# Optimization experiments

Measured on AMD Instinct MI355X. Metric: run time of the kernel, lower is better.

Reference implementation:

```python
import jax, jax.numpy as jnp
import numpy as np

B, N, E, H = 4, 512, 512, 8   # batch, tokens, embedding_channels (=KV_size_S), num_heads
C = 4 * E                      # KV_size_C
D = E // H                     # head dim
EPS = 1e-5                     # InstanceNorm2d default eps


def _inorm(x, axes):
    # InstanceNorm2d (affine=False): normalize over spatial axes with biased variance
    m = jnp.mean(x, axis=axes, keepdims=True)
    v = jnp.var(x, axis=axes, keepdims=True)
    return (x - m) * jax.lax.rsqrt(v + EPS)


def setup_inputs() -> dict:
    key = jax.random.key(0)
    ks = jax.random.split(key, 24)
    s = 0.02
    inp = {
        'emb1': jax.random.normal(ks[0], (B, N, E), jnp.float32),
        'emb2': jax.random.normal(ks[1], (B, N, E), jnp.float32),
        'emb3': jax.random.normal(ks[2], (B, N, E), jnp.float32),
        'emb4': jax.random.normal(ks[3], (B, N, E), jnp.float32),
        'emb_C': jax.random.normal(ks[4], (B, N, C), jnp.float32),
        'Wq1': jax.random.normal(ks[5], (E, E), jnp.float32) * s,
        'Wq2': jax.random.normal(ks[6], (E, E), jnp.float32) * s,
        'Wq3': jax.random.normal(ks[7], (E, E), jnp.float32) * s,
        'Wq4': jax.random.normal(ks[8], (E, E), jnp.float32) * s,
        'Wk': jax.random.normal(ks[9], (E, E), jnp.float32) * s,
        'Wv': jax.random.normal(ks[10], (E, E), jnp.float32) * s,
        'WqC': jax.random.normal(ks[11], (C, C), jnp.float32) * s,
        'WkC': jax.random.normal(ks[12], (C, C), jnp.float32) * s,
        'WvC': jax.random.normal(ks[13], (C, C), jnp.float32) * s,
        'Wo1': jax.random.normal(ks[14], (E, E), jnp.float32) * s,
        'Wo2': jax.random.normal(ks[15], (E, E), jnp.float32) * s,
        'Wo3': jax.random.normal(ks[16], (E, E), jnp.float32) * s,
        'Wo4': jax.random.normal(ks[17], (E, E), jnp.float32) * s,
    }
    return inp


def _heads(x):
    # [B, N, E] -> [B, H, N, D]
    b, n, _ = x.shape
    return x.reshape(b, n, H, D).transpose(0, 2, 1, 3)


def reference(emb1, emb2, emb3, emb4, emb_C,
              Wq1, Wq2, Wq3, Wq4, Wk, Wv, WqC, WkC, WvC,
              Wo1, Wo2, Wo3, Wo4):
    # ---- channel cross-attention ----
    QC = emb_C @ WqC.T            # [B, N, C]
    KC = emb_C @ WkC.T
    VC = emb_C @ WvC.T
    attn_c = jnp.einsum('bnc,bnd->bcd', QC, KC)        # [B, C, C]
    sim_c = jax.nn.softmax(_inorm(attn_c, (1, 2)), axis=-1)  # psi1 + softmax(dim=3)
    ctx_c = jnp.einsum('bcd,bnd->bcn', sim_c, VC)      # [B, C, N]
    T_hat = ctx_c.transpose(0, 2, 1)                   # [B, N, C]
    # split last dim into 4 chunks of E, concat along tokens -> [B, 4N, E]
    KV_S = jnp.concatenate(jnp.split(T_hat, 4, axis=2), axis=1)

    # ---- spatial multi-head cross-attention, shared K/V ----
    K = _heads(KV_S @ Wk.T)       # [B, H, 4N, D]
    V = _heads(KV_S @ Wv.T)

    outs = []
    for emb, Wq, Wo in ((emb1, Wq1, Wo1), (emb2, Wq2, Wo2),
                        (emb3, Wq3, Wo3), (emb4, Wq4, Wo4)):
        Q = _heads(emb @ Wq.T)                          # [B, H, N, D]
        attn = jnp.einsum('bhnd,bhmd->bhnm', Q, K)      # [B, H, N, 4N]
        sim = jax.nn.softmax(_inorm(attn, (2, 3)), axis=-1)  # psi2 + softmax
        ctx = jnp.einsum('bhnm,bhmd->bhnd', sim, V)     # [B, H, N, D]
        ctx = ctx.transpose(0, 2, 1, 3).reshape(emb.shape[0], emb.shape[1], E)
        outs.append(ctx @ Wo.T)
    return tuple(outs)
```

## Files before the change

### kernel.cpp

```cpp
#include <hip/hip_runtime.h>
#include <hip/hip_bf16.h>
#include <hip/hip_fp16.h>

typedef long long i64;
typedef unsigned int u32;
typedef __attribute__((ext_vector_type(8))) short bf16x8;
typedef __attribute__((ext_vector_type(4))) float f32x4;

#define MFMA_BF16 __builtin_amdgcn_mfma_f32_16x16x32_bf16

__device__ __forceinline__ void glds16(const void* g, void* l){
    __builtin_amdgcn_global_load_lds((const __attribute__((address_space(1))) u32*)g,
                                     (__attribute__((address_space(3))) u32*)l, 16, 0, 0);
}
__device__ __forceinline__ void split1(float x, ushort& h, ushort& l){
    unsigned b = __float_as_uint(x);
    h = (ushort)(b >> 16);
    float hf = __uint_as_float(b & 0xFFFF0000u);
    float lf = x - hf;
    l = (ushort)(__float_as_uint(lf) >> 16);
}
__device__ __forceinline__ float bfpair(ushort h, ushort l){
    return __uint_as_float((u32)h << 16) + __uint_as_float((u32)l << 16);
}
__device__ __forceinline__ void ld4h(const __half* p, float v[4]){
    const __half2* q = (const __half2*)p;
    __half2 a = q[0], b = q[1];
    v[0]=__low2float(a); v[1]=__high2float(a);
    v[2]=__low2float(b); v[3]=__high2float(b);
}
__device__ __forceinline__ bf16x8 fragS(const ushort* P, int row, int g){
    return *(const bf16x8*)&P[row*64 + (((g) ^ (row & 7)) << 3)];
}

struct P4 { const void* p[4]; };
struct I4 { int v[4]; };

struct PSJobs { const float* s[13]; ushort* d[13]; int st[14]; };
__global__ __launch_bounds__(256) void presplit(PSJobs J){
    int bid = blockIdx.x, j = 0;
    while (bid >= J.st[j+1]) ++j;
    i64 base = (i64)(bid - J.st[j])*2048 + threadIdx.x*8;
    i64 loOff = (i64)(J.st[j+1] - J.st[j])*2048;
    const float* sp = J.s[j]; ushort* dp = J.d[j];
    float4 a = *(const float4*)&sp[base];
    float4 b = *(const float4*)&sp[base+4];
    float v[8] = {a.x,a.y,a.z,a.w,b.x,b.y,b.z,b.w};
    ushort h[8], l[8];
    #pragma unroll
    for (int t = 0; t < 8; ++t) split1(v[t], h[t], l[t]);
    *(ushort4*)&dp[base]         = make_ushort4(h[0],h[1],h[2],h[3]);
    *(ushort4*)&dp[base+4]       = make_ushort4(h[4],h[5],h[6],h[7]);
    *(ushort4*)&dp[loOff+base]   = make_ushort4(l[0],l[1],l[2],l[3]);
    *(ushort4*)&dp[loOff+base+4] = make_ushort4(l[4],l[5],l[6],l[7]);
}

template<bool AF16, int OUT>
__global__ __launch_bounds__(256) void gemm_ps(
    P4 Ap, P4 Bp, P4 Cp, I4 cmode, float* __restrict__ stats,
    int K, int zdiv,
    i64 ab2, i64 alda, i64 aLo,
    i64 bb2, i64 bldb, i64 bLo,
    i64 cb2, i64 cld, i64 cLo)
{
    __shared__ ushort Ah[4096], Al[4096], Bh[4096], Bl[4096];
    __shared__ float sred[4], qred[4];
    const int z = blockIdx.z, z1 = z / zdiv, z2 = z % zdiv;
    const int m0 = blockIdx.y*128, n0 = blockIdx.x*128;
    const int tid = threadIdx.x, lane = tid & 63, wid = tid >> 6;
    const int wm = wid >> 1, wn = wid & 1, fr = lane & 15, kc = lane >> 4;
    const ushort* Aps = (const ushort*)Ap.p[z1] + (i64)z2*ab2 + (i64)m0*alda;
    const __half* Af  = (const __half*)Ap.p[z1] + (i64)z2*ab2 + (i64)m0*alda;
    const ushort* Bps = (const ushort*)Bp.p[z1] + (i64)z2*bb2 + (i64)n0*bldb;

    f32x4 acc[4][4];
    #pragma unroll
    for (int i = 0; i < 4; ++i)
        #pragma unroll
        for (int j = 0; j < 4; ++j) acc[i][j] = (f32x4){0.f,0.f,0.f,0.f};

    for (int k0 = 0; k0 < K; k0 += 32) {
        if (!AF16) {
            #pragma unroll
            for (int q = 0; q < 2; ++q) {
                int r = wid*32 + q*16 + (lane>>2);
                const ushort* sp = Aps + (i64)r*alda + k0 + (lane&3)*8;
                glds16(sp,       &Ah[(wid*32+q*16)*32]);
                glds16(sp + aLo, &Al[(wid*32+q*16)*32]);
            }
        } else {
            #pragma unroll
            for (int s4 = 0; s4 < 4; ++s4) {
                int v = tid + s4*256; int r = v >> 3, c4 = v & 7;
                float vals[4]; ld4h(&Af[(i64)r*alda + k0 + c4*4], vals);
                ushort h[4], l[4];
                #pragma unroll
                for (int t = 0; t < 4; ++t) split1(vals[t], h[t], l[t]);
                *(ushort4*)&Ah[r*32 + c4*4] = make_ushort4(h[0],h[1],h[2],h[3]);
                *(ushort4*)&Al[r*32 + c4*4] = make_ushort4(l[0],l[1],l[2],l[3]);
            }
        }
        #pragma unroll
        for (int q = 0; q < 2; ++q) {
            int r = wid*32 + q*16 + (lane>>2);
            const ushort* sp = Bps + (i64)r*bldb + k0 + (lane&3)*8;
            glds16(sp,       &Bh[(wid*32+q*16)*32]);
            glds16(sp + bLo, &Bl[(wid*32+q*16)*32]);
        }
        __syncthreads();
        bf16x8 a_h[4], a_l[4], b_h[4], b_l[4];
        #pragma unroll
        for (int i = 0; i < 4; ++i) {
            int row = wm*64 + i*16 + fr;
            a_h[i] = *(const bf16x8*)&Ah[row*32 + kc*8];
            a_l[i] = *(const bf16x8*)&Al[row*32 + kc*8];
        }
        #pragma unroll
        for (int j = 0; j < 4; ++j) {
            int row = wn*64 + j*16 + fr;
            b_h[j] = *(const bf16x8*)&Bh[row*32 + kc*8];
            b_l[j] = *(const bf16x8*)&Bl[row*32 + kc*8];
        }
        #pragma unroll
        for (int i = 0; i < 4; ++i)
            #pragma unroll
            for (int j = 0; j < 4; ++j) {
                acc[i][j] = MFMA_BF16(a_h[i], b_h[j], acc[i][j], 0, 0, 0);
                acc[i][j] = MFMA_BF16(a_h[i], b_l[j], acc[i][j], 0, 0, 0);
                acc[i][j] = MFMA_BF16(a_l[i], b_h[j], acc[i][j], 0, 0, 0);
            }
        __syncthreads();
    }

    const i64 cbase = (i64)z2*cb2;
    if (OUT == 0) {
        float* C = (float*)Cp.p[z1];
        #pragma unroll
        for (int i = 0; i < 4; ++i)
            #pragma unroll
            for (int j = 0; j < 4; ++j)
                #pragma unroll
                for (int r = 0; r < 4; ++r) {
                    int m = m0 + wm*64 + i*16 + kc*4 + r;
                    int n = n0 + wn*64 + j*16 + fr;
                    C[cbase + (i64)m*cld + n] = acc[i][j][r];
                }
    } else if (OUT == 1) {
        ushort* C = (ushort*)Cp.p[z1];
        const int cfg = cmode.v[z1];
        const int tr = cfg >> 30;
        const i64 ldv = cfg & 0x3FFFFFFF;
        #pragma unroll
        for (int i = 0; i < 4; ++i)
            #pragma unroll
            for (int j = 0; j < 4; ++j)
                #pragma unroll
                for (int r = 0; r < 4; ++r) {
                    int m = m0 + wm*64 + i*16 + kc*4 + r;
                    int n = n0 + wn*64 + j*16 + fr;
                    ushort h, l; split1(acc[i][j][r], h, l);
                    i64 off = cbase + (tr ? (i64)n*ldv + m : (i64)m*ldv + n);
                    C[off] = h; C[off + cLo] = l;
                }
    } else if (OUT == 2) {
        __half* C = (__half*)Cp.p[z1];
        float ls = 0.f, lq = 0.f;
        #pragma unroll
        for (int i = 0; i < 4; ++i)
            #pragma unroll
            for (int j = 0; j < 4; ++j)
                #pragma unroll
                for (int r = 0; r < 4; ++r) {
                    int m = m0 + wm*64 + i*16 + kc*4 + r;
                    int n = n0 + wn*64 + j*16 + fr;
                    float v = acc[i][j][r];
                    ls += v; lq += v*v;
                    C[cbase + (i64)m*cld + n] = __float2half(v);
                }
        #pragma unroll
        for (int off = 32; off; off >>= 1) { ls += __shfl_xor(ls, off); lq += __shfl_xor(lq, off); }
        if (lane == 0) { sred[wid] = ls; qred[wid] = lq; }
        __syncthreads();
        if (tid == 0) {
            atomicAdd(&stats[2*z],   sred[0]+sred[1]+sred[2]+sred[3]);
            atomicAdd(&stats[2*z+1], qred[0]+qred[1]+qred[2]+qred[3]);
        }
    } else {
        ushort* C = (ushort*)Cp.p[z1];
        #pragma unroll
        for (int i = 0; i < 4; ++i)
            #pragma unroll
            for (int j = 0; j < 4; ++j)
                #pragma unroll
                for (int r = 0; r < 4; ++r) {
                    int m = m0 + wm*64 + i*16 + kc*4 + r;
                    int n = n0 + wn*64 + j*16 + fr;
                    ushort h, l; split1(acc[i][j][r], h, l);
                    i64 off = cbase + ((i64)(m >> 9) << 18) + ((i64)n << 9) + (m & 511);
                    C[off] = h; C[off + cLo] = l;
                }
    }
}

__global__ __launch_bounds__(256) void softmax_rows(
    __half* __restrict__ attn, const float* __restrict__ stats,
    int rows_per_stat, float inv_count)
{
    const int ROWLEN = 2048;
    const int row = blockIdx.x;
    const int sidx = row / rows_per_stat;
    float sm = stats[2*sidx], sq = stats[2*sidx+1];
    float mean = sm * inv_count;
    float var = fmaxf(sq * inv_count - mean*mean, 0.f);
    float scale = rsqrtf(var + 1e-5f);
    __half* rp = attn + (i64)row * ROWLEN;
    const int tid = threadIdx.x;
    float v[8]; float mx = -3.4e38f;
    #pragma unroll
    for (int s = 0; s < 8; ++s) { float x = __half2float(rp[tid + s*256]) * scale; v[s] = x; mx = fmaxf(mx, x); }
    #pragma unroll
    for (int off = 32; off; off >>= 1) mx = fmaxf(mx, __shfl_xor(mx, off));
    __shared__ float red[4];
    if ((tid & 63) == 0) red[tid >> 6] = mx;
    __syncthreads();
    mx = fmaxf(fmaxf(red[0], red[1]), fmaxf(red[2], red[3]));
    float ls = 0.f;
    #pragma unroll
    for (int s = 0; s < 8; ++s) { float e = __expf(v[s] - mx); v[s] = e; ls += e; }
    #pragma unroll
    for (int off = 32; off; off >>= 1) ls += __shfl_xor(ls, off);
    __syncthreads();
    if ((tid & 63) == 0) red[tid >> 6] = ls;
    __syncthreads();
    float inv = 1.f / (red[0] + red[1] + red[2] + red[3]);
    #pragma unroll
    for (int s = 0; s < 8; ++s) rp[tid + s*256] = __float2half(v[s] * inv);
}

__global__ __launch_bounds__(256) void gram64(
    const ushort* __restrict__ hi, i64 loOff, float* __restrict__ parts,
    i64 bstride, i64 zs2)
{
    __shared__ float T[16][68];
    __shared__ float csred[4][64];
    const int z = blockIdx.x;
    const int tid = threadIdx.x;
    const ushort* base = hi + (i64)(z>>3)*bstride + (i64)blockIdx.z*zs2
                       + (i64)blockIdx.y*256*512 + (z&7)*64;
    float g[4][4] = {{0.f}};
    float cs = 0.f;
    const int sr = tid >> 4, sc = (tid & 15) * 4;
    const int col = tid & 63, qq = tid >> 6;
    for (int grp = 0; grp < 16; ++grp) {
        i64 idx = (i64)(grp*16 + sr)*512 + sc;
        ushort4 hv = *(const ushort4*)&base[idx];
        ushort4 lv = *(const ushort4*)&base[loOff + idx];
        float4 ld;
        ld.x = bfpair(hv.x, lv.x); ld.y = bfpair(hv.y, lv.y);
        ld.z = bfpair(hv.z, lv.z); ld.w = bfpair(hv.w, lv.w);
        __syncthreads();
        *(float4*)&T[sr][sc] = ld;
        __syncthreads();
        #pragma unroll
        for (int rr = 0; rr < 16; ++rr) {
            const float4 a = *(const float4*)&T[rr][sr*4];
            const float4 b = *(const float4*)&T[rr][sc];
            g[0][0]+=a.x*b.x; g[0][1]+=a.x*b.y; g[0][2]+=a.x*b.z; g[0][3]+=a.x*b.w;
            g[1][0]+=a.y*b.x; g[1][1]+=a.y*b.y; g[1][2]+=a.y*b.z; g[1][3]+=a.y*b.w;
            g[2][0]+=a.z*b.x; g[2][1]+=a.z*b.y; g[2][2]+=a.z*b.z; g[2][3]+=a.z*b.w;
            g[3][0]+=a.w*b.x; g[3][1]+=a.w*b.y; g[3][2]+=a.w*b.z; g[3][3]+=a.w*b.w;
        }
        cs += T[qq*4+0][col] + T[qq*4+1][col] + T[qq*4+2][col] + T[qq*4+3][col];
    }
    float* outp = parts + (i64)((blockIdx.z*gridDim.y + blockIdx.y)*gridDim.x + blockIdx.x)*4160;
    #pragma unroll
    for (int x = 0; x < 4; ++x)
        #pragma unroll
        for (int y = 0; y < 4; ++y)
            outp[(sr*4+x)*64 + sc + y] = g[x][y];
    csred[qq][col] = cs;
    __syncthreads();
    if (tid < 64) outp[4096 + tid] = csred[0][tid]+csred[1][tid]+csred[2][tid]+csred[3][tid];
}

__global__ __launch_bounds__(256) void fin_stats(
    const float* __restrict__ gq, const float* __restrict__ gk,
    float* __restrict__ ss)
{
    const int z = blockIdx.x, s = blockIdx.y;
    const int tid = threadIdx.x;
    const int lane = tid & 63, wid = tid >> 6;
    const float* q0 = gq + (i64)((s*2+0)*32 + z)*4160;
    const float* q1 = gq + (i64)((s*2+1)*32 + z)*4160;
    float p2 = 0.f;
    for (int i = tid; i < 4096; i += 256) {
        float a = q0[i] + q1[i];
        float b = 0.f;
        #pragma unroll
        for (int c = 0; c < 8; ++c) b += gk[(i64)(c*32 + z)*4160 + i];
        p2 += a*b;
    }
    float p1 = 0.f;
    if (tid < 64) {
        float a = q0[4096+tid] + q1[4096+tid];
        float b = 0.f;
        #pragma unroll
        for (int c = 0; c < 8; ++c) b += gk[(i64)(c*32 + z)*4160 + 4096 + tid];
        p1 = a*b;
    }
    #pragma unroll
    for (int off = 32; off; off >>= 1) { p2 += __shfl_xor(p2, off); p1 += __shfl_xor(p1, off); }
    __shared__ float r2[4], r1[4];
    if (lane == 0) { r2[wid] = p2; r1[wid] = p1; }
    __syncthreads();
    if (tid == 0) {
        float S2 = r2[0]+r2[1]+r2[2]+r2[3];
        float S1 = r1[0]+r1[1]+r1[2]+r1[3];
        const float inv = 1.f/1048576.f;
        float mu = S1*inv;
        float var = fmaxf(S2*inv - mu*mu, 0.f);
        float sc = rsqrtf(var + 1e-5f);
        ss[(s*32+z)*2] = sc;
        ss[(s*32+z)*2+1] = sc*mu;
    }
}

__global__ __launch_bounds__(256) void flash_ps(
    const ushort* __restrict__ Qp, const ushort* __restrict__ Kp,
    const ushort* __restrict__ Vtp, const float* __restrict__ ss,
    ushort* __restrict__ ctxp)
{
    __shared__ ushort QPh[4096], QPl[4096];
    __shared__ ushort Kh[4096], Kl[4096];
    __shared__ ushort Vh[2][4096], Vl[2][4096];
    __shared__ float denl[2][64];
    const int qt = blockIdx.x, zz = blockIdx.y, s = blockIdx.z;
    const int b = zz >> 3, hD = (zz & 7) * 64;
    const float scale = ss[(s*32+zz)*2], shift = ss[(s*32+zz)*2+1];
    const ushort* Qb = Qp + (i64)s*2097152 + (i64)b*262144 + (i64)(qt*64)*512 + hD;
    const ushort* Kb = Kp + (i64)b*1048576 + hD;
    const ushort* Vb = Vtp + (i64)b*1048576 + (i64)hD*2048;
    const int tid = threadIdx.x, lane = tid & 63, wid = tid >> 6;
    const int wq = wid >> 1, wk = wid & 1, fr = lane & 15, kc = lane >> 4;

    auto stage64 = [&](const ushort* src, i64 ld, i64 lo, ushort* Lh, ushort* Ll){
        #pragma unroll
        for (int q = 0; q < 2; ++q) {
            int rb = wid*16 + q*8;
            int r = rb + (lane >> 3);
            int gs = (lane & 7) ^ (r & 7);
            const ushort* p = src + (i64)r*ld + gs*8;
            glds16(p,      &Lh[rb*64]);
            glds16(p + lo, &Ll[rb*64]);
        }
    };

    stage64(Qb, 512, 1048576, QPh, QPl);
    stage64(Kb, 512, 4194304, Kh, Kl);
    stage64(Vb, 2048, 4194304, Vh[0], Vl[0]);
    __syncthreads();

    bf16x8 qh[2][2], ql[2][2];
    #pragma unroll
    for (int i = 0; i < 2; ++i)
        #pragma unroll
        for (int ks = 0; ks < 2; ++ks) {
            int row = wq*32 + i*16 + fr;
            qh[i][ks] = fragS(QPh, row, ks*4 + kc);
            ql[i][ks] = fragS(QPl, row, ks*4 + kc);
        }
    __syncthreads();

    f32x4 ctx[2][2];
    #pragma unroll
    for (int i = 0; i < 2; ++i)
        #pragma unroll
        for (int j = 0; j < 2; ++j) ctx[i][j] = (f32x4){0.f,0.f,0.f,0.f};
    float den_lr[2][4] = {{0.f}};

    for (int t = 0; t < 32; ++t) {
        f32x4 sacc[2][2];
        #pragma unroll
        for (int i = 0; i < 2; ++i)
            #pragma unroll
            for (int j = 0; j < 2; ++j) sacc[i][j] = (f32x4){0.f,0.f,0.f,0.f};
        #pragma unroll
        for (int ks = 0; ks < 2; ++ks) {
            bf16x8 khf[2], klf[2];
            #pragma unroll
            for (int j = 0; j < 2; ++j) {
                int row = wk*32 + j*16 + fr;
                khf[j] = fragS(Kh, row, ks*4 + kc);
                klf[j] = fragS(Kl, row, ks*4 + kc);
            }
            #pragma unroll
            for (int i = 0; i < 2; ++i)
                #pragma unroll
                for (int j = 0; j < 2; ++j) {
                    sacc[i][j] = MFMA_BF16(qh[i][ks], khf[j], sacc[i][j], 0, 0, 0);
                    sacc[i][j] = MFMA_BF16(qh[i][ks], klf[j], sacc[i][j], 0, 0, 0);
                    sacc[i][j] = MFMA_BF16(ql[i][ks], khf[j], sacc[i][j], 0, 0, 0);
                }
        }
        #pragma unroll
        for (int i = 0; i < 2; ++i)
            #pragma unroll
            for (int j = 0; j < 2; ++j)
                #pragma unroll
                for (int r = 0; r < 4; ++r) {
                    float p = __expf(sacc[i][j][r]*scale - shift);
                    den_lr[i][r] += p;
                    ushort h, l; split1(p, h, l);
                    int row = wq*32 + i*16 + kc*4 + r;
                    int col = wk*32 + j*16 + fr;
                    int pos = row*64 + ((((col>>3) ^ (row&7)) << 3) | (col & 7));
                    QPh[pos] = h; QPl[pos] = l;
                }
        __syncthreads();
        if (t + 1 < 32) {
            stage64(Kb + (i64)((t+1)*64)*512, 512, 4194304, Kh, Kl);
            stage64(Vb + (t+1)*64, 2048, 4194304, Vh[(t+1)&1], Vl[(t+1)&1]);
        }
        #pragma unroll
        for (int ks = 0; ks < 2; ++ks) {
            bf16x8 vhf[2], vlf[2], pah[2], pal[2];
            #pragma unroll
            for (int j = 0; j < 2; ++j) {
                int row = wk*32 + j*16 + fr;
                vhf[j] = fragS(Vh[t&1], row, ks*4 + kc);
                vlf[j] = fragS(Vl[t&1], row, ks*4 + kc);
            }
            #pragma unroll
            for (int i = 0; i < 2; ++i) {
                int row = wq*32 + i*16 + fr;
                pah[i] = fragS(QPh, row, ks*4 + kc);
                pal[i] = fragS(QPl, row, ks*4 + kc);
            }
            #pragma unroll
            for (int i = 0; i < 2; ++i)
                #pragma unroll
                for (int j = 0; j < 2; ++j) {
                    ctx[i][j] = MFMA_BF16(pah[i], vhf[j], ctx[i][j], 0, 0, 0);
                    ctx[i][j] = MFMA_BF16(pah[i], vlf[j], ctx[i][j], 0, 0, 0);
                    ctx[i][j] = MFMA_BF16(pal[i], vhf[j], ctx[i][j], 0, 0, 0);
                }
        }
        __syncthreads();
    }

    #pragma unroll
    for (int i = 0; i < 2; ++i)
        #pragma unroll
        for (int r = 0; r < 4; ++r) {
            float d = den_lr[i][r];
            d += __shfl_xor(d, 1); d += __shfl_xor(d, 2);
            d += __shfl_xor(d, 4); d += __shfl_xor(d, 8);
            if (fr == 0) denl[wk][wq*32 + i*16 + kc*4 + r] = d;
        }
    __syncthreads();
    ushort* Cb = ctxp + (i64)s*2097152 + (i64)b*262144;
    #pragma unroll
    for (int i = 0; i < 2; ++i)
        #pragma unroll
        for (int j = 0; j < 2; ++j)
            #pragma unroll
            for (int r = 0; r < 4; ++r) {
                int row = wq*32 + i*16 + kc*4 + r;
                int col = wk*32 + j*16 + fr;
                float dv = denl[0][row] + denl[1][row];
                ushort h, l; split1(ctx[i][j][r] / dv, h, l);
                i64 off = (i64)(qt*64 + row)*512 + hD + col;
                Cb[off] = h; Cb[off + 1048576] = l;
            }
}

static inline P4 p4x(const void* a, const void* b, const void* c, const void* d){
    P4 x; x.p[0]=a; x.p[1]=b; x.p[2]=c; x.p[3]=d; return x;
}
static inline P4 p4x(const void* a){ return p4x(a,a,a,a); }
static inline I4 i4x(int a, int b, int c, int d){ I4 x; x.v[0]=a; x.v[1]=b; x.v[2]=c; x.v[3]=d; return x; }
#define TRC(ld) ((1<<30)|(ld))

extern "C" void kernel_launch(void* const* d_in, const int* in_sizes, int n_in,
                              void* d_out, int out_size, void* d_ws, size_t ws_size,
                              hipStream_t stream)
{
    (void)in_sizes; (void)n_in; (void)out_size;
    const float* emb[4] = {(const float*)d_in[0], (const float*)d_in[1],
                           (const float*)d_in[2], (const float*)d_in[3]};
    const float* embC = (const float*)d_in[4];
    const float* Wq[4] = {(const float*)d_in[5], (const float*)d_in[6],
                          (const float*)d_in[7], (const float*)d_in[8]};
    const float* Wk  = (const float*)d_in[9];
    const float* Wv  = (const float*)d_in[10];
    const float* WqC = (const float*)d_in[11];
    const float* WkC = (const float*)d_in[12];
    const float* WvC = (const float*)d_in[13];
    const float* Wo[4] = {(const float*)d_in[14], (const float*)d_in[15],
                          (const float*)d_in[16], (const float*)d_in[17]};
    float* out = (float*)d_out;

    char* ws = (char*)d_ws;
    const size_t MB = 1024*1024;
    if (ws_size < 128*MB + 512) return;
    auto U = [&](size_t mb){ return (ushort*)(ws + mb*MB); };
    float* stats = (float*)(ws + 122*MB);
    float* ssbuf = (float*)(ws + 122*MB + 1024);
    float* GKp   = (float*)(ws + 48*MB);
    float* GQp   = (float*)(ws + 53*MB);
    __half* scores = (__half*)(ws + 16*MB);

    hipMemsetAsync(stats, 0, 512, stream);

    {
        PSJobs J;
        const float* srcs[13] = {embC, WqC, WkC, WvC, Wk, Wv,
                                 Wq[0],Wq[1],Wq[2],Wq[3], Wo[0],Wo[1],Wo[2]};
        ushort* dsts[13] = {U(0),U(16),U(32),U(48),U(64),U(65),
                            U(66),U(67),U(68),U(69), U(70),U(71),U(72)};
        int blks[13] = {2048,2048,2048,2048,128,128, 128,128,128,128, 128,128,128};
        int a = 0;
        for (int j = 0; j < 13; ++j) { J.s[j]=srcs[j]; J.d[j]=dsts[j]; J.st[j]=a; a+=blks[j]; }
        J.st[13] = a;
        presplit<<<dim3(a), 256, 0, stream>>>(J);
    }
    gemm_ps<false,1><<<dim3(16, 4, 12), 256, 0, stream>>>(
        p4x(U(0)), p4x(U(16), U(32), U(48), U(48)), p4x(U(74), U(90), U(106), U(106)),
        i4x(TRC(512), TRC(512), 2048, 2048), nullptr, 2048, 4,
        1048576, 2048, 4194304,   0, 2048, 4194304,   1048576, 0, 4194304);
    {
        PSJobs J;
        const float* srcs[13] = {emb[0], emb[1], emb[2], emb[3], Wo[3],
                                 nullptr,nullptr,nullptr,nullptr,nullptr,nullptr,nullptr,nullptr};
        ushort* dsts[13] = {U(0), U(4), U(8), U(12), U(73),
                            nullptr,nullptr,nullptr,nullptr,nullptr,nullptr,nullptr,nullptr};
        int blks[5] = {512,512,512,512,128};
        int a = 0;
        for (int j = 0; j < 5; ++j) { J.s[j]=srcs[j]; J.d[j]=dsts[j]; J.st[j]=a; a+=blks[j]; }
        for (int j = 5; j < 14; ++j) J.st[j] = a;
        presplit<<<dim3(a), 256, 0, stream>>>(J);
    }
    gemm_ps<false,2><<<dim3(16, 16, 4), 256, 0, stream>>>(
        p4x(U(74)), p4x(U(90)), p4x(scores), i4x(0,0,0,0), stats, 512, 4,
        1048576, 512, 4194304,   1048576, 512, 4194304,   4194304, 2048, 0);
    softmax_rows<<<dim3(4*2048), 256, 0, stream>>>(scores, stats, 2048, 1.f/4194304.f);
    gemm_ps<true,3><<<dim3(4, 16, 4), 256, 0, stream>>>(
        p4x(scores), p4x(U(106)), p4x(U(48)), i4x(0,0,0,0), nullptr, 2048, 4,
        4194304, 2048, 0,   1048576, 2048, 4194304,   1048576, 0, 4194304);
    gemm_ps<false,1><<<dim3(4, 16, 8), 256, 0, stream>>>(
        p4x(U(48)), p4x(U(64), U(65), U(65), U(65)), p4x(U(74), U(90), U(90), U(90)),
        i4x(512, TRC(2048), 0, 0), nullptr, 512, 4,
        1048576, 512, 4194304,   0, 512, 262144,   1048576, 0, 4194304);
    gemm_ps<false,1><<<dim3(4, 4, 16), 256, 0, stream>>>(
        p4x(U(0), U(4), U(8), U(12)), p4x(U(66), U(67), U(68), U(69)),
        p4x(U(106), U(110), U(114), U(118)),
        i4x(512,512,512,512), nullptr, 512, 4,
        262144, 512, 1048576,   0, 512, 262144,   262144, 0, 1048576);
    gram64<<<dim3(32, 8, 1), 256, 0, stream>>>(U(74), 4194304, GKp, 1048576, 0);
    gram64<<<dim3(32, 2, 4), 256, 0, stream>>>(U(106), 1048576, GQp, 262144, 2097152);
    fin_stats<<<dim3(32, 4), 256, 0, stream>>>(GQp, GKp, ssbuf);
    flash_ps<<<dim3(8, 32, 4), 256, 0, stream>>>(U(106), U(74), U(90), ssbuf, U(16));
    gemm_ps<false,0><<<dim3(4, 4, 16), 256, 0, stream>>>(
        p4x(U(16), U(20), U(24), U(28)), p4x(U(70), U(71), U(72), U(73)),
        p4x(out, out + 1048576, out + 2097152, out + 3145728),
        i4x(0,0,0,0), nullptr, 512, 4,
        262144, 512, 1048576,   0, 512, 262144,   262144, 512, 1048576);
}
```

Measured before the change: 739.4 us.

## Double-buffer GEMM LDS tiles and XOR-swizzle to avoid bank conflicts

```diff
diff --git a/kernel.cpp b/kernel.cpp
--- a/kernel.cpp
+++ b/kernel.cpp
@@ -63,7 +63,7 @@
     i64 bb2, i64 bldb, i64 bLo,
     i64 cb2, i64 cld, i64 cLo)
 {
-    __shared__ ushort Ah[4096], Al[4096], Bh[4096], Bl[4096];
+    __shared__ ushort Ah[2][4096], Al[2][4096], Bh[2][4096], Bl[2][4096];
     __shared__ float sred[4], qred[4];
     const int z = blockIdx.z, z1 = z / zdiv, z2 = z % zdiv;
     const int m0 = blockIdx.y*128, n0 = blockIdx.x*128;
@@ -73,20 +73,28 @@
     const __half* Af  = (const __half*)Ap.p[z1] + (i64)z2*ab2 + (i64)m0*alda;
     const ushort* Bps = (const ushort*)Bp.p[z1] + (i64)z2*bb2 + (i64)n0*bldb;
 
-    f32x4 acc[4][4];
-    #pragma unroll
-    for (int i = 0; i < 4; ++i)
-        #pragma unroll
-        for (int j = 0; j < 4; ++j) acc[i][j] = (f32x4){0.f,0.f,0.f,0.f};
-
-    for (int k0 = 0; k0 < K; k0 += 32) {
+    const int srow = wid*32 + (lane >> 2);
+    const int sg   = lane & 3;
+
+    auto stageB = [&](int k0, int pb){
+        #pragma unroll
+        for (int q = 0; q < 2; ++q) {
+            int r  = srow + q*16;
+            int gs = sg ^ ((r >> 1) & 3);
+            const ushort* sp = Bps + (i64)r*bldb + k0 + gs*8;
+            glds16(sp,       &Bh[pb][(wid*32+q*16)*32]);
+            glds16(sp + bLo, &Bl[pb][(wid*32+q*16)*32]);
+        }
+    };
+    auto stageA = [&](int k0, int pb){
         if (!AF16) {
             #pragma unroll
             for (int q = 0; q < 2; ++q) {
-                int r = wid*32 + q*16 + (lane>>2);
-                const ushort* sp = Aps + (i64)r*alda + k0 + (lane&3)*8;
-                glds16(sp,       &Ah[(wid*32+q*16)*32]);
-                glds16(sp + aLo, &Al[(wid*32+q*16)*32]);
+                int r  = srow + q*16;
+                int gs = sg ^ ((r >> 1) & 3);
+                const ushort* sp = Aps + (i64)r*alda + k0 + gs*8;
+                glds16(sp,       &Ah[pb][(wid*32+q*16)*32]);
+                glds16(sp + aLo, &Al[pb][(wid*32+q*16)*32]);
             }
         } else {
             #pragma unroll
@@ -96,30 +104,44 @@
                 ushort h[4], l[4];
                 #pragma unroll
                 for (int t = 0; t < 4; ++t) split1(vals[t], h[t], l[t]);
-                *(ushort4*)&Ah[r*32 + c4*4] = make_ushort4(h[0],h[1],h[2],h[3]);
-                *(ushort4*)&Al[r*32 + c4*4] = make_ushort4(l[0],l[1],l[2],l[3]);
-            }
-        }
-        #pragma unroll
-        for (int q = 0; q < 2; ++q) {
-            int r = wid*32 + q*16 + (lane>>2);
-            const ushort* sp = Bps + (i64)r*bldb + k0 + (lane&3)*8;
-            glds16(sp,       &Bh[(wid*32+q*16)*32]);
-            glds16(sp + bLo, &Bl[(wid*32+q*16)*32]);
-        }
-        __syncthreads();
+                int pc = ((((c4 >> 1) ^ ((r >> 1) & 3)) << 1) | (c4 & 1)) * 4;
+                *(ushort4*)&Ah[pb][r*32 + pc] = make_ushort4(h[0],h[1],h[2],h[3]);
+                *(ushort4*)&Al[pb][r*32 + pc] = make_ushort4(l[0],l[1],l[2],l[3]);
+            }
+        }
+    };
+    auto rd = [&](const ushort* P, int row, int kcc)->bf16x8 {
+        return *(const bf16x8*)&P[row*32 + ((kcc ^ ((row >> 1) & 3)) << 3)];
+    };
+
+    f32x4 acc[4][4];
+    #pragma unroll
+    for (int i = 0; i < 4; ++i)
+        #pragma unroll
+        for (int j = 0; j < 4; ++j) acc[i][j] = (f32x4){0.f,0.f,0.f,0.f};
+
+    const int NT = K >> 5;
+    stageA(0, 0); stageB(0, 0);
+    __syncthreads();
+
+    for (int t = 0; t < NT; ++t) {
+        const int cur = t & 1;
+        if (t + 1 < NT) {
+            stageA((t+1) << 5, cur ^ 1);
+            stageB((t+1) << 5, cur ^ 1);
+        }
         bf16x8 a_h[4], a_l[4], b_h[4], b_l[4];
         #pragma unroll
         for (int i = 0; i < 4; ++i) {
             int row = wm*64 + i*16 + fr;
-            a_h[i] = *(const bf16x8*)&Ah[row*32 + kc*8];
-            a_l[i] = *(const bf16x8*)&Al[row*32 + kc*8];
+            a_h[i] = rd(Ah[cur], row, kc);
+            a_l[i] = rd(Al[cur], row, kc);
         }
         #pragma unroll
         for (int j = 0; j < 4; ++j) {
             int row = wn*64 + j*16 + fr;
-            b_h[j] = *(const bf16x8*)&Bh[row*32 + kc*8];
-            b_l[j] = *(const bf16x8*)&Bl[row*32 + kc*8];
+            b_h[j] = rd(Bh[cur], row, kc);
+            b_l[j] = rd(Bl[cur], row, kc);
         }
         #pragma unroll
         for (int i = 0; i < 4; ++i)
```

After: 708.5 us. 1.04x faster.
